# Kernel optimization log

Hardware: AMD Instinct MI355X
Metric: run time of the kernel (lower is better)

Reference implementation:

```python
import jax, jax.numpy as jnp
import numpy as np

NEG_SLOPE = 0.2  # keras 'leaky_relu' default negative slope

def _leaky_relu(t):
    return jnp.where(t >= 0, t, NEG_SLOPE * t)

def setup_inputs() -> dict:
    key = jax.random.key(0)
    kx, kq, kk, kv, ko, kg = jax.random.split(key, 6)
    B, H, W, C, A = 4, 64, 64, 256, 128
    x = jax.random.normal(kx, (B, H, W, C), dtype=jnp.float32)
    # 1x1 conv kernels == [Cin, Cout] matrices; glorot-normal-ish scaling
    Wq = jax.random.normal(kq, (C, A), dtype=jnp.float32) * (2.0 / (C + A)) ** 0.5
    Wk = jax.random.normal(kk, (C, A), dtype=jnp.float32) * (2.0 / (C + A)) ** 0.5
    Wv = jax.random.normal(kv, (C, A), dtype=jnp.float32) * (2.0 / (C + A)) ** 0.5
    Wo = jax.random.normal(ko, (A, C), dtype=jnp.float32) * (2.0 / (A + C)) ** 0.5
    # ChannelLearnableMultiplier weight: truncated_normal(0, 0.01) ~ small values near 0
    w_gamma = jax.random.normal(kg, (1, 1, 1, C), dtype=jnp.float32) * 0.01
    return {"x": x, "Wq": Wq, "Wk": Wk, "Wv": Wv, "Wo": Wo, "w_gamma": w_gamma}

def reference(x, Wq, Wk, Wv, Wo, w_gamma):
    B, H, W, C = x.shape
    A = Wq.shape[1]
    # 1x1 conv projections with leaky_relu activation, flatten spatial -> [B, N, A]
    q = _leaky_relu(jnp.einsum('bhwc,ca->bhwa', x, Wq)).reshape(B, H * W, A)
    k = _leaky_relu(jnp.einsum('bhwc,ca->bhwa', x, Wk)).reshape(B, H * W, A)
    v = _leaky_relu(jnp.einsum('bhwc,ca->bhwa', x, Wv)).reshape(B, H * W, A)
    # keras Attention(use_scale=False, score_mode='dot'): softmax(q k^T) v
    scores = jnp.einsum('bnd,bmd->bnm', q, k)          # [B, N, N]
    attn = jax.nn.softmax(scores, axis=-1)
    o = jnp.einsum('bnm,bmd->bnd', attn, v)            # [B, N, A]
    o = o.reshape(B, H, W, A)
    # output 1x1 conv, linear activation
    y = jnp.einsum('bhwa,ac->bhwc', o, Wo)
    # ChannelLearnableMultiplier: tanh(relu(1 + w)) * y
    return jnp.tanh(jax.nn.relu(1.0 + w_gamma)) * y
```

## Files before the change

kernel.cpp:

```cpp
#include <hip/hip_runtime.h>
#include <hip/hip_bf16.h>
#include <cstdint>
#include <cstddef>

typedef __bf16 bf16x8 __attribute__((ext_vector_type(8)));
typedef _Float16 f16x8 __attribute__((ext_vector_type(8)));
typedef short short8 __attribute__((ext_vector_type(8)));
typedef short short4v __attribute__((ext_vector_type(4)));
typedef float f32x4 __attribute__((ext_vector_type(4)));

__device__ __forceinline__ unsigned short f2bf(float f) {
    union { float f; uint32_t u; } v; v.f = f;
    uint32_t u = v.u;
    return (unsigned short)((u + 0x7FFFu + ((u >> 16) & 1u)) >> 16);
}
__device__ __forceinline__ float bf2f(unsigned short h) {
    union { uint32_t u; float f; } v; v.u = ((uint32_t)h) << 16;
    return v.f;
}
__device__ __forceinline__ unsigned short f2h(float f) {
    union { _Float16 h; unsigned short u; } v; v.h = (_Float16)f;
    return v.u;
}

__global__ __launch_bounds__(256) void qkv_kernel(
    const float* __restrict__ x,
    const float* __restrict__ Wq,
    const float* __restrict__ Wk,
    const float* __restrict__ Wv,
    unsigned short* __restrict__ qkv_ws)
{
    const int rowtile = blockIdx.x;
    const int proj    = blockIdx.y;
    const float* W = (proj == 0) ? Wq : ((proj == 1) ? Wk : Wv);
    unsigned short* outqk = qkv_ws + (size_t)proj * 2097152u;
    unsigned short* vt    = qkv_ws + (size_t)2 * 2097152u;
    const bool need_lo = (proj < 2);

    const int tid  = threadIdx.x;
    const int lane = tid & 63, wave = tid >> 6;
    const int lo   = lane & 15, quad = lane >> 4;

    __shared__ __align__(16) unsigned short Xh[64][72], Xl[64][72];
    __shared__ __align__(16) unsigned short Wh[128][72], Wl[128][72];

    f32x4 acc[8];
    #pragma unroll
    for (int i = 0; i < 8; ++i) acc[i] = (f32x4){0.f, 0.f, 0.f, 0.f};

    for (int kc = 0; kc < 4; ++kc) {
        __syncthreads();
        #pragma unroll
        for (int i = 0; i < 4; ++i) {
            int flat4 = (i * 256 + tid) * 4;
            int row = flat4 >> 6, col = flat4 & 63;
            float4 t = *(const float4*)(x + (size_t)(rowtile * 64 + row) * 256 + kc * 64 + col);
            short4v h, l;
            float tv[4] = {t.x, t.y, t.z, t.w};
            #pragma unroll
            for (int j = 0; j < 4; ++j) {
                unsigned short hj = f2bf(tv[j]);
                h[j] = (short)hj;
                l[j] = (short)f2bf(tv[j] - bf2f(hj));
            }
            *(short4v*)(&Xh[row][col]) = h;
            if (need_lo) *(short4v*)(&Xl[row][col]) = l;
        }
        {
            int n = tid & 127;
            for (int g = (tid >> 7); g < 16; g += 2) {
                int k0 = g * 4;
                short4v h, l;
                #pragma unroll
                for (int j = 0; j < 4; ++j) {
                    float wv = W[(size_t)(kc * 64 + k0 + j) * 128 + n];
                    unsigned short hj = f2bf(wv);
                    h[j] = (short)hj;
                    l[j] = (short)f2bf(wv - bf2f(hj));
                }
                *(short4v*)(&Wh[n][k0]) = h;
                if (need_lo) *(short4v*)(&Wl[n][k0]) = l;
            }
        }
        __syncthreads();
        #pragma unroll
        for (int ks = 0; ks < 2; ++ks) {
            bf16x8 ah = *(const bf16x8*)(&Xh[wave * 16 + lo][ks * 32 + quad * 8]);
            #pragma unroll
            for (int nb = 0; nb < 8; ++nb) {
                bf16x8 bh = *(const bf16x8*)(&Wh[nb * 16 + lo][ks * 32 + quad * 8]);
                acc[nb] = __builtin_amdgcn_mfma_f32_16x16x32_bf16(ah, bh, acc[nb], 0, 0, 0);
                if (need_lo) {
                    bf16x8 al = *(const bf16x8*)(&Xl[wave * 16 + lo][ks * 32 + quad * 8]);
                    bf16x8 bl = *(const bf16x8*)(&Wl[nb * 16 + lo][ks * 32 + quad * 8]);
                    acc[nb] = __builtin_amdgcn_mfma_f32_16x16x32_bf16(al, bh, acc[nb], 0, 0, 0);
                    acc[nb] = __builtin_amdgcn_mfma_f32_16x16x32_bf16(ah, bl, acc[nb], 0, 0, 0);
                }
            }
        }
    }
    if (proj < 2) {
        #pragma unroll
        for (int nb = 0; nb < 8; ++nb) {
            #pragma unroll
            for (int r = 0; r < 4; ++r) {
                float v = acc[nb][r];
                v = (v >= 0.f) ? v : 0.2f * v;
                int m = rowtile * 64 + wave * 16 + quad * 4 + r;
                outqk[(size_t)m * 128 + nb * 16 + lo] = f2h(v);
            }
        }
    } else {
        const int b   = rowtile >> 6;
        const int sb  = (rowtile & 63) * 64;
        #pragma unroll
        for (int nb = 0; nb < 8; ++nb) {
            #pragma unroll
            for (int r = 0; r < 4; ++r) {
                float v = acc[nb][r];
                v = (v >= 0.f) ? v : 0.2f * v;
                int seq = sb + wave * 16 + quad * 4 + r;
                int d   = nb * 16 + lo;
                vt[(size_t)b * 524288 + (size_t)d * 4096 + seq] = f2bf(v);
            }
        }
    }
}

__global__ __launch_bounds__(256) void attn_kernel(
    const unsigned short* __restrict__ qkv_ws,
    unsigned short* __restrict__ part,
    float* __restrict__ lpart,
    int chunk)
{
    const int b  = blockIdx.x;
    const int qt = blockIdx.y;
    const int z  = blockIdx.z;
    const int tid  = threadIdx.x;
    const int lane = tid & 63, wave = tid >> 6;
    const int lo   = lane & 15, quad = lane >> 4;

    const unsigned short* q  = qkv_ws;
    const unsigned short* k  = qkv_ws + 2097152u;
    const unsigned short* vt = qkv_ws + (size_t)2 * 2097152u + (size_t)b * 524288u;

    __shared__ __align__(16) unsigned short Ks[32][136];
    __shared__ __align__(16) unsigned short Vt[128][40];
    __shared__ __align__(16) unsigned short Ps[4][16][40];

    f16x8 qf[4];
    #pragma unroll
    for (int ks = 0; ks < 4; ++ks)
        qf[ks] = *(const f16x8*)(q + ((size_t)(b * 4096 + qt * 64 + wave * 16 + lo)) * 128
                                   + ks * 32 + quad * 8);

    f32x4 oacc[8];
    #pragma unroll
    for (int i = 0; i < 8; ++i) oacc[i] = (f32x4){0.f, 0.f, 0.f, 0.f};
    float lsum[4] = {1e-30f, 1e-30f, 1e-30f, 1e-30f};

    const float LOG2E  = 1.44269504088896f;
    const float NSHIFT = -40.0f * 1.44269504088896f;

    const int niter = chunk >> 5;
    for (int kt = 0; kt < niter; ++kt) {
        const int s0 = z * chunk + kt * 32;
        __syncthreads();
        #pragma unroll
        for (int i = 0; i < 2; ++i) {
            int flat = (i * 256 + tid) * 8;
            int row = flat >> 7, col = flat & 127;
            *(short8*)(&Ks[row][col]) =
                *(const short8*)(k + ((size_t)(b * 4096 + s0 + row)) * 128 + col);
        }
        #pragma unroll
        for (int i = 0; i < 2; ++i) {
            int flat = (i * 256 + tid) * 8;
            int d = flat >> 5, sc = flat & 31;
            *(short8*)(&Vt[d][sc]) = *(const short8*)(vt + (size_t)d * 4096 + s0 + sc);
        }
        __syncthreads();

        f32x4 s[2];
        s[0] = (f32x4){0.f, 0.f, 0.f, 0.f};
        s[1] = (f32x4){0.f, 0.f, 0.f, 0.f};
        #pragma unroll
        for (int ks = 0; ks < 4; ++ks) {
            #pragma unroll
            for (int nb = 0; nb < 2; ++nb) {
                f16x8 bf = *(const f16x8*)(&Ks[nb * 16 + lo][ks * 32 + quad * 8]);
                s[nb] = __builtin_amdgcn_mfma_f32_16x16x32_f16(qf[ks], bf, s[nb], 0, 0, 0);
            }
        }
        #pragma unroll
        for (int nb = 0; nb < 2; ++nb) {
            #pragma unroll
            for (int r = 0; r < 4; ++r) {
                float t = fminf(fmaf(s[nb][r], LOG2E, NSHIFT), 125.0f);
                float p = exp2f(t);
                lsum[r] += p;
                Ps[wave][quad * 4 + r][nb * 16 + lo] = f2bf(p);
            }
        }
        bf16x8 pf = *(const bf16x8*)(&Ps[wave][lo][quad * 8]);
        #pragma unroll
        for (int nb = 0; nb < 8; ++nb) {
            bf16x8 vf = *(const bf16x8*)(&Vt[nb * 16 + lo][quad * 8]);
            oacc[nb] = __builtin_amdgcn_mfma_f32_16x16x32_bf16(pf, vf, oacc[nb], 0, 0, 0);
        }
    }

    #pragma unroll
    for (int r = 0; r < 4; ++r) {
        float xr = lsum[r];
        #pragma unroll
        for (int m = 1; m < 16; m <<= 1) xr += __shfl_xor(xr, m, 64);
        lsum[r] = xr;
    }
    #pragma unroll
    for (int nb = 0; nb < 8; ++nb) {
        #pragma unroll
        for (int r = 0; r < 4; ++r) {
            int m = b * 4096 + qt * 64 + wave * 16 + quad * 4 + r;
            part[((size_t)z * 16384 + m) * 128 + nb * 16 + lo] = f2bf(oacc[nb][r]);
        }
    }
    if (lo == 0) {
        #pragma unroll
        for (int r = 0; r < 4; ++r) {
            int m = b * 4096 + qt * 64 + wave * 16 + quad * 4 + r;
            lpart[(size_t)z * 16384 + m] = lsum[r];
        }
    }
}

__global__ __launch_bounds__(256) void outproj_kernel(
    const unsigned short* __restrict__ part,
    const float* __restrict__ lpart,
    const float* __restrict__ Wo,
    const float* __restrict__ wg,
    float* __restrict__ out,
    int nsplit)
{
    const int rowtile = blockIdx.x;
    const int ch      = blockIdx.y;
    const int tid  = threadIdx.x;
    const int lane = tid & 63, wave = tid >> 6;
    const int lo   = lane & 15, quad = lane >> 4;

    __shared__ __align__(16) unsigned short Os[64][136];
    __shared__ __align__(16) unsigned short WoT[128][136];

    #pragma unroll
    for (int i = 0; i < 4; ++i) {
        int flat = (i * 256 + tid) * 8;
        int row = flat >> 7, col = flat & 127;
        int m = rowtile * 64 + row;
        float acc8[8] = {0.f, 0.f, 0.f, 0.f, 0.f, 0.f, 0.f, 0.f};
        float l = 0.f;
        for (int z = 0; z < nsplit; ++z) {
            short8 t = *(const short8*)(part + ((size_t)z * 16384 + m) * 128 + col);
            #pragma unroll
            for (int j = 0; j < 8; ++j) acc8[j] += bf2f((unsigned short)t[j]);
            l += lpart[(size_t)z * 16384 + m];
        }
        float inv = 1.0f / l;
        short8 o8;
        #pragma unroll
        for (int j = 0; j < 8; ++j) o8[j] = (short)f2bf(acc8[j] * inv);
        *(short8*)(&Os[row][col]) = o8;
    }
    {
        int c = tid & 127;
        for (int g = (tid >> 7); g < 16; g += 2) {
            int a0 = g * 8;
            short8 t;
            #pragma unroll
            for (int j = 0; j < 8; ++j)
                t[j] = (short)f2bf(Wo[(size_t)(a0 + j) * 256 + ch * 128 + c]);
            *(short8*)(&WoT[c][a0]) = t;
        }
    }
    __syncthreads();

    f32x4 acc[8];
    #pragma unroll
    for (int i = 0; i < 8; ++i) acc[i] = (f32x4){0.f, 0.f, 0.f, 0.f};
    #pragma unroll
    for (int ks = 0; ks < 4; ++ks) {
        bf16x8 a = *(const bf16x8*)(&Os[wave * 16 + lo][ks * 32 + quad * 8]);
        #pragma unroll
        for (int nb = 0; nb < 8; ++nb) {
            bf16x8 bf = *(const bf16x8*)(&WoT[nb * 16 + lo][ks * 32 + quad * 8]);
            acc[nb] = __builtin_amdgcn_mfma_f32_16x16x32_bf16(a, bf, acc[nb], 0, 0, 0);
        }
    }
    #pragma unroll
    for (int nb = 0; nb < 8; ++nb) {
        int c = ch * 128 + nb * 16 + lo;
        float g = 1.0f + wg[c];
        if (g < 0.f) g = 0.f;
        g = tanhf(g);
        #pragma unroll
        for (int r = 0; r < 4; ++r) {
            int m = rowtile * 64 + wave * 16 + quad * 4 + r;
            out[(size_t)m * 256 + c] = acc[nb][r] * g;
        }
    }
}

extern "C" void kernel_launch(void* const* d_in, const int* in_sizes, int n_in,
                              void* d_out, int out_size, void* d_ws, size_t ws_size,
                              hipStream_t stream) {
    const float* x  = (const float*)d_in[0];
    const float* Wq = (const float*)d_in[1];
    const float* Wk = (const float*)d_in[2];
    const float* Wv = (const float*)d_in[3];
    const float* Wo = (const float*)d_in[4];
    const float* wg = (const float*)d_in[5];
    float* out = (float*)d_out;

    unsigned short* ws = (unsigned short*)d_ws;
    const int nsplit = (ws_size >= (size_t)30000000) ? 4 : 2;
    unsigned short* part  = ws + (size_t)3 * 2097152u;
    float*          lpart = (float*)(ws + (size_t)(3 + nsplit) * 2097152u);
    const int chunk = 4096 / nsplit;

    qkv_kernel<<<dim3(256, 3), 256, 0, stream>>>(x, Wq, Wk, Wv, ws);
    attn_kernel<<<dim3(4, 64, nsplit), 256, 0, stream>>>(ws, part, lpart, chunk);
    outproj_kernel<<<dim3(256, 2), 256, 0, stream>>>(part, lpart, Wo, wg, out, nsplit);
}
```

Baseline: 204.2 us.

## Pre-convert weights, double query rows per wave, prefetch K/V tiles, raise split count

A new prep kernel converts and transposes the projection weights (hi/lo bf16 split) and Wo into bf16 once, so the qkv and outproj kernels load ready-made weights instead of converting them per block. The attention kernel now gives each wave 32 query rows, reusing every K/V tile for two MFMA groups, and loads the next K/V tile into registers while computing on the current one. P is truncated to bf16 rather than rounded, and the sequence split count is raised (8 or 4 depending on workspace size). This adds a launch and reuses the partial buffer for the weight scratch, and it increases register pressure in the attention kernel.

```diff
diff --git a/kernel.cpp b/kernel.cpp
--- a/kernel.cpp
+++ b/kernel.cpp
@@ -23,16 +23,59 @@
     return v.u;
 }
 
+__global__ __launch_bounds__(256) void prep_kernel(
+    const float* __restrict__ Wq, const float* __restrict__ Wk,
+    const float* __restrict__ Wv, const float* __restrict__ Wo,
+    unsigned short* __restrict__ wt_hi,
+    unsigned short* __restrict__ wt_lo,
+    unsigned short* __restrict__ wot)
+{
+    const int bid = blockIdx.x, t = threadIdx.x;
+    __shared__ __align__(16) unsigned short Th[128][72], Tl[128][72];
+    __shared__ __align__(16) unsigned short T[64][136];
+    if (bid < 12) {
+        const int proj = bid >> 2, kc = bid & 3;
+        const float* W = (proj == 0) ? Wq : ((proj == 1) ? Wk : Wv);
+        for (int r = 0; r < 32; ++r) {
+            int idx = r * 256 + t;
+            int kk = idx >> 7, n = idx & 127;
+            float w = W[(size_t)(kc * 64 + kk) * 128 + n];
+            unsigned short h = f2bf(w);
+            Th[n][kk] = h;
+            Tl[n][kk] = f2bf(w - bf2f(h));
+        }
+        __syncthreads();
+        int n = t >> 1, k0 = (t & 1) * 32;
+        size_t off = (size_t)proj * 32768 + (size_t)kc * 8192 + (size_t)n * 64 + k0;
+        #pragma unroll
+        for (int j = 0; j < 4; ++j) {
+            *(short8*)(wt_hi + off + j * 8) = *(const short8*)(&Th[n][k0 + j * 8]);
+            *(short8*)(wt_lo + off + j * 8) = *(const short8*)(&Tl[n][k0 + j * 8]);
+        }
+    } else if (bid < 16) {
+        const int c0 = (bid - 12) * 64;
+        for (int r = 0; r < 32; ++r) {
+            int idx = r * 256 + t;
+            int a = idx >> 6, cc = idx & 63;
+            T[cc][a] = f2bf(Wo[(size_t)a * 256 + c0 + cc]);
+        }
+        __syncthreads();
+        int cc = t >> 2, a0 = (t & 3) * 32;
+        #pragma unroll
+        for (int j = 0; j < 4; ++j)
+            *(short8*)(wot + (size_t)(c0 + cc) * 128 + a0 + j * 8) =
+                *(const short8*)(&T[cc][a0 + j * 8]);
+    }
+}
+
 __global__ __launch_bounds__(256) void qkv_kernel(
     const float* __restrict__ x,
-    const float* __restrict__ Wq,
-    const float* __restrict__ Wk,
-    const float* __restrict__ Wv,
+    const unsigned short* __restrict__ wt_hi,
+    const unsigned short* __restrict__ wt_lo,
     unsigned short* __restrict__ qkv_ws)
 {
     const int rowtile = blockIdx.x;
     const int proj    = blockIdx.y;
-    const float* W = (proj == 0) ? Wq : ((proj == 1) ? Wk : Wv);
     unsigned short* outqk = qkv_ws + (size_t)proj * 2097152u;
     unsigned short* vt    = qkv_ws + (size_t)2 * 2097152u;
     const bool need_lo = (proj < 2);
@@ -48,15 +91,17 @@
     #pragma unroll
     for (int i = 0; i < 8; ++i) acc[i] = (f32x4){0.f, 0.f, 0.f, 0.f};
 
+    const int wn = tid >> 1, wk0 = (tid & 1) * 32;
+
     for (int kc = 0; kc < 4; ++kc) {
         __syncthreads();
         #pragma unroll
         for (int i = 0; i < 4; ++i) {
             int flat4 = (i * 256 + tid) * 4;
             int row = flat4 >> 6, col = flat4 & 63;
-            float4 t = *(const float4*)(x + (size_t)(rowtile * 64 + row) * 256 + kc * 64 + col);
+            float4 tv4 = *(const float4*)(x + (size_t)(rowtile * 64 + row) * 256 + kc * 64 + col);
+            float tv[4] = {tv4.x, tv4.y, tv4.z, tv4.w};
             short4v h, l;
-            float tv[4] = {t.x, t.y, t.z, t.w};
             #pragma unroll
             for (int j = 0; j < 4; ++j) {
                 unsigned short hj = f2bf(tv[j]);
@@ -67,19 +112,14 @@
             if (need_lo) *(short4v*)(&Xl[row][col]) = l;
         }
         {
-            int n = tid & 127;
-            for (int g = (tid >> 7); g < 16; g += 2) {
-                int k0 = g * 4;
-                short4v h, l;
+            const size_t off = (size_t)proj * 32768 + (size_t)kc * 8192 + (size_t)wn * 64 + wk0;
+            #pragma unroll
+            for (int j = 0; j < 4; ++j)
+                *(short8*)(&Wh[wn][wk0 + j * 8]) = *(const short8*)(wt_hi + off + j * 8);
+            if (need_lo) {
                 #pragma unroll
-                for (int j = 0; j < 4; ++j) {
-                    float wv = W[(size_t)(kc * 64 + k0 + j) * 128 + n];
-                    unsigned short hj = f2bf(wv);
-                    h[j] = (short)hj;
-                    l[j] = (short)f2bf(wv - bf2f(hj));
-                }
-                *(short4v*)(&Wh[n][k0]) = h;
-                if (need_lo) *(short4v*)(&Wl[n][k0]) = l;
+                for (int j = 0; j < 4; ++j)
+                    *(short8*)(&Wl[wn][wk0 + j * 8]) = *(const short8*)(wt_lo + off + j * 8);
             }
         }
         __syncthreads();
@@ -111,8 +151,8 @@
             }
         }
     } else {
-        const int b   = rowtile >> 6;
-        const int sb  = (rowtile & 63) * 64;
+        const int b  = rowtile >> 6;
+        const int sb = (rowtile & 63) * 64;
         #pragma unroll
         for (int nb = 0; nb < 8; ++nb) {
             #pragma unroll
@@ -146,90 +186,125 @@
 
     __shared__ __align__(16) unsigned short Ks[32][136];
     __shared__ __align__(16) unsigned short Vt[128][40];
-    __shared__ __align__(16) unsigned short Ps[4][16][40];
-
-    f16x8 qf[4];
-    #pragma unroll
-    for (int ks = 0; ks < 4; ++ks)
-        qf[ks] = *(const f16x8*)(q + ((size_t)(b * 4096 + qt * 64 + wave * 16 + lo)) * 128
-                                   + ks * 32 + quad * 8);
-
-    f32x4 oacc[8];
-    #pragma unroll
-    for (int i = 0; i < 8; ++i) oacc[i] = (f32x4){0.f, 0.f, 0.f, 0.f};
-    float lsum[4] = {1e-30f, 1e-30f, 1e-30f, 1e-30f};
+    __shared__ __align__(16) unsigned short Ps[4][32][40];
+
+    const int qbase = qt * 128 + wave * 32;
+    f16x8 qf[2][4];
+    #pragma unroll
+    for (int g = 0; g < 2; ++g)
+        #pragma unroll
+        for (int ks = 0; ks < 4; ++ks)
+            qf[g][ks] = *(const f16x8*)(q + ((size_t)(b * 4096 + qbase + g * 16 + lo)) * 128
+                                          + ks * 32 + quad * 8);
+
+    f32x4 oacc[2][8];
+    #pragma unroll
+    for (int g = 0; g < 2; ++g)
+        #pragma unroll
+        for (int i = 0; i < 8; ++i) oacc[g][i] = (f32x4){0.f, 0.f, 0.f, 0.f};
+    float lsum[2][4];
+    #pragma unroll
+    for (int g = 0; g < 2; ++g)
+        #pragma unroll
+        for (int r = 0; r < 4; ++r) lsum[g][r] = 1e-30f;
 
     const float LOG2E  = 1.44269504088896f;
     const float NSHIFT = -40.0f * 1.44269504088896f;
 
+    const int c0 = tid, c1 = 256 + tid;
+    const int krow0 = c0 >> 4, kcol0 = (c0 & 15) * 8;
+    const int krow1 = (c1 - 256) >> 4 + 0;
+    const int vd0 = c0 >> 2, vs0 = (c0 & 3) * 8;
+    const int vd1 = (c1 - 256) >> 2, vs1 = ((c1 - 256) & 3) * 8;
+    const int krow1b = 16 + (tid >> 4), kcol1b = (tid & 15) * 8;
+    const int vd1b = 64 + (tid >> 2), vs1b = (tid & 3) * 8;
+    (void)krow1; (void)vd1; (void)vs1; (void)c1;
+
     const int niter = chunk >> 5;
+    const int sbase = z * chunk;
+
+    short8 ka, kb, va, vb;
+    {
+        ka = *(const short8*)(k + ((size_t)(b * 4096 + sbase + krow0)) * 128 + kcol0);
+        kb = *(const short8*)(k + ((size_t)(b * 4096 + sbase + krow1b)) * 128 + kcol1b);
+        va = *(const short8*)(vt + (size_t)vd0 * 4096 + sbase + vs0);
+        vb = *(const short8*)(vt + (size_t)vd1b * 4096 + sbase + vs1b);
+    }
+
     for (int kt = 0; kt < niter; ++kt) {
-        const int s0 = z * chunk + kt * 32;
-        __syncthreads();
-        #pragma unroll
-        for (int i = 0; i < 2; ++i) {
-            int flat = (i * 256 + tid) * 8;
-            int row = flat >> 7, col = flat & 127;
-            *(short8*)(&Ks[row][col]) =
-                *(const short8*)(k + ((size_t)(b * 4096 + s0 + row)) * 128 + col);
-        }
-        #pragma unroll
-        for (int i = 0; i < 2; ++i) {
-            int flat = (i * 256 + tid) * 8;
-            int d = flat >> 5, sc = flat & 31;
-            *(short8*)(&Vt[d][sc]) = *(const short8*)(vt + (size_t)d * 4096 + s0 + sc);
-        }
-        __syncthreads();
-
-        f32x4 s[2];
-        s[0] = (f32x4){0.f, 0.f, 0.f, 0.f};
-        s[1] = (f32x4){0.f, 0.f, 0.f, 0.f};
+        __syncthreads();
+        *(short8*)(&Ks[krow0][kcol0]) = ka;
+        *(short8*)(&Ks[krow1b][kcol1b]) = kb;
+        *(short8*)(&Vt[vd0][vs0]) = va;
+        *(short8*)(&Vt[vd1b][vs1b]) = vb;
+        __syncthreads();
+        if (kt + 1 < niter) {
+            const int s1 = sbase + (kt + 1) * 32;
+            ka = *(const short8*)(k + ((size_t)(b * 4096 + s1 + krow0)) * 128 + kcol0);
+            kb = *(const short8*)(k + ((size_t)(b * 4096 + s1 + krow1b)) * 128 + kcol1b);
+            va = *(const short8*)(vt + (size_t)vd0 * 4096 + s1 + vs0);
+            vb = *(const short8*)(vt + (size_t)vd1b * 4096 + s1 + vs1b);
+        }
+
+        f32x4 s[2][2];
+        s[0][0] = (f32x4){0.f,0.f,0.f,0.f}; s[0][1] = (f32x4){0.f,0.f,0.f,0.f};
+        s[1][0] = (f32x4){0.f,0.f,0.f,0.f}; s[1][1] = (f32x4){0.f,0.f,0.f,0.f};
         #pragma unroll
         for (int ks = 0; ks < 4; ++ks) {
             #pragma unroll
             for (int nb = 0; nb < 2; ++nb) {
                 f16x8 bf = *(const f16x8*)(&Ks[nb * 16 + lo][ks * 32 + quad * 8]);
-                s[nb] = __builtin_amdgcn_mfma_f32_16x16x32_f16(qf[ks], bf, s[nb], 0, 0, 0);
-            }
-        }
-        #pragma unroll
-        for (int nb = 0; nb < 2; ++nb) {
-            #pragma unroll
-            for (int r = 0; r < 4; ++r) {
-                float t = fminf(fmaf(s[nb][r], LOG2E, NSHIFT), 125.0f);
-                float p = exp2f(t);
-                lsum[r] += p;
-                Ps[wave][quad * 4 + r][nb * 16 + lo] = f2bf(p);
-            }
-        }
-        bf16x8 pf = *(const bf16x8*)(&Ps[wave][lo][quad * 8]);
+                s[0][nb] = __builtin_amdgcn_mfma_f32_16x16x32_f16(qf[0][ks], bf, s[0][nb], 0, 0, 0);
+                s[1][nb] = __builtin_amdgcn_mfma_f32_16x16x32_f16(qf[1][ks], bf, s[1][nb], 0, 0, 0);
+            }
+        }
+        #pragma unroll
+        for (int g = 0; g < 2; ++g) {
+            #pragma unroll
+            for (int nb = 0; nb < 2; ++nb) {
+                #pragma unroll
+                for (int r = 0; r < 4; ++r) {
+                    float t = fminf(fmaf(s[g][nb][r], LOG2E, NSHIFT), 125.0f);
+                    union { float f; uint32_t u; } pv; pv.f = exp2f(t);
+                    unsigned short pt = (unsigned short)(pv.u >> 16);
+                    lsum[g][r] += bf2f(pt);
+                    Ps[wave][g * 16 + quad * 4 + r][nb * 16 + lo] = pt;
+                }
+            }
+        }
+        bf16x8 pf0 = *(const bf16x8*)(&Ps[wave][lo][quad * 8]);
+        bf16x8 pf1 = *(const bf16x8*)(&Ps[wave][16 + lo][quad * 8]);
         #pragma unroll
         for (int nb = 0; nb < 8; ++nb) {
             bf16x8 vf = *(const bf16x8*)(&Vt[nb * 16 + lo][quad * 8]);
-            oacc[nb] = __builtin_amdgcn_mfma_f32_16x16x32_bf16(pf, vf, oacc[nb], 0, 0, 0);
-        }
-    }
-
-    #pragma unroll
-    for (int r = 0; r < 4; ++r) {
-        float xr = lsum[r];
-        #pragma unroll
-        for (int m = 1; m < 16; m <<= 1) xr += __shfl_xor(xr, m, 64);
-        lsum[r] = xr;
-    }
-    #pragma unroll
-    for (int nb = 0; nb < 8; ++nb) {
+            oacc[0][nb] = __builtin_amdgcn_mfma_f32_16x16x32_bf16(pf0, vf, oacc[0][nb], 0, 0, 0);
+            oacc[1][nb] = __builtin_amdgcn_mfma_f32_16x16x32_bf16(pf1, vf, oacc[1][nb], 0, 0, 0);
+        }
+    }
+
+    #pragma unroll
+    for (int g = 0; g < 2; ++g) {
         #pragma unroll
         for (int r = 0; r < 4; ++r) {
-            int m = b * 4096 + qt * 64 + wave * 16 + quad * 4 + r;
-            part[((size_t)z * 16384 + m) * 128 + nb * 16 + lo] = f2bf(oacc[nb][r]);
-        }
-    }
-    if (lo == 0) {
-        #pragma unroll
-        for (int r = 0; r < 4; ++r) {
-            int m = b * 4096 + qt * 64 + wave * 16 + quad * 4 + r;
-            lpart[(size_t)z * 16384 + m] = lsum[r];
+            float xr = lsum[g][r];
+            #pragma unroll
+            for (int m = 1; m < 16; m <<= 1) xr += __shfl_xor(xr, m, 64);
+            lsum[g][r] = xr;
+        }
+        #pragma unroll
+        for (int nb = 0; nb < 8; ++nb) {
+            #pragma unroll
+            for (int r = 0; r < 4; ++r) {
+                int m = b * 4096 + qbase + g * 16 + quad * 4 + r;
+                part[((size_t)z * 16384 + m) * 128 + nb * 16 + lo] = f2bf(oacc[g][nb][r]);
+            }
+        }
+        if (lo == 0) {
+            #pragma unroll
+            for (int r = 0; r < 4; ++r) {
+                int m = b * 4096 + qbase + g * 16 + quad * 4 + r;
+                lpart[(size_t)z * 16384 + m] = lsum[g][r];
+            }
         }
     }
 }
@@ -237,7 +312,7 @@
 __global__ __launch_bounds__(256) void outproj_kernel(
     const unsigned short* __restrict__ part,
     const float* __restrict__ lpart,
-    const float* __restrict__ Wo,
+    const unsigned short* __restrict__ wot,
     const float* __restrict__ wg,
     float* __restrict__ out,
     int nsplit)
@@ -256,13 +331,13 @@
         int flat = (i * 256 + tid) * 8;
         int row = flat >> 7, col = flat & 127;
         int m = rowtile * 64 + row;
-        float acc8[8] = {0.f, 0.f, 0.f, 0.f, 0.f, 0.f, 0.f, 0.f};
+        float acc8[8] = {0.f,0.f,0.f,0.f,0.f,0.f,0.f,0.f};
         float l = 0.f;
-        for (int z = 0; z < nsplit; ++z) {
-            short8 t = *(const short8*)(part + ((size_t)z * 16384 + m) * 128 + col);
+        for (int zz = 0; zz < nsplit; ++zz) {
+            short8 t = *(const short8*)(part + ((size_t)zz * 16384 + m) * 128 + col);
             #pragma unroll
             for (int j = 0; j < 8; ++j) acc8[j] += bf2f((unsigned short)t[j]);
-            l += lpart[(size_t)z * 16384 + m];
+            l += lpart[(size_t)zz * 16384 + m];
         }
         float inv = 1.0f / l;
         short8 o8;
@@ -271,15 +346,11 @@
         *(short8*)(&Os[row][col]) = o8;
     }
     {
-        int c = tid & 127;
-        for (int g = (tid >> 7); g < 16; g += 2) {
-            int a0 = g * 8;
-            short8 t;
-            #pragma unroll
-            for (int j = 0; j < 8; ++j)
-                t[j] = (short)f2bf(Wo[(size_t)(a0 + j) * 256 + ch * 128 + c]);
-            *(short8*)(&WoT[c][a0]) = t;
-        }
+        int c = tid >> 1, a0 = (tid & 1) * 64;
+        #pragma unroll
+        for (int j = 0; j < 8; ++j)
+            *(short8*)(&WoT[c][a0 + j * 8]) =
+                *(const short8*)(wot + (size_t)(ch * 128 + c) * 128 + a0 + j * 8);
     }
     __syncthreads();
 
@@ -321,12 +392,18 @@
     float* out = (float*)d_out;
 
     unsigned short* ws = (unsigned short*)d_ws;
-    const int nsplit = (ws_size >= (size_t)30000000) ? 4 : 2;
-    unsigned short* part  = ws + (size_t)3 * 2097152u;
-    float*          lpart = (float*)(ws + (size_t)(3 + nsplit) * 2097152u);
+    const int nsplit = (ws_size >= (size_t)47000000) ? 8 : 4;
     const int chunk = 4096 / nsplit;
 
-    qkv_kernel<<<dim3(256, 3), 256, 0, stream>>>(x, Wq, Wk, Wv, ws);
-    attn_kernel<<<dim3(4, 64, nsplit), 256, 0, stream>>>(ws, part, lpart, chunk);
-    outproj_kernel<<<dim3(256, 2), 256, 0, stream>>>(part, lpart, Wo, wg, out, nsplit);
-}
+    unsigned short* qkv_ws = ws;
+    unsigned short* part   = ws + (size_t)3 * 2097152u;
+    unsigned short* wt_hi  = part;
+    unsigned short* wt_lo  = part + 98304u;
+    float* lpart = (float*)(part + (size_t)nsplit * 2097152u);
+    unsigned short* wot = (unsigned short*)(lpart + (size_t)nsplit * 16384u);
+
+    prep_kernel<<<dim3(16), 256, 0, stream>>>(Wq, Wk, Wv, Wo, wt_hi, wt_lo, wot);
+    qkv_kernel<<<dim3(256, 3), 256, 0, stream>>>(x, wt_hi, wt_lo, qkv_ws);
+    attn_kernel<<<dim3(4, 32, nsplit), 256, 0, stream>>>(qkv_ws, part, lpart, chunk);
+    outproj_kernel<<<dim3(256, 2), 256, 0, stream>>>(part, lpart, wot, wg, out, nsplit);
+}
```

Measured after the change: 178.6 us. -12.5%, faster.
